# Optimization experiments

Measured on AMD Instinct MI355X. Metric: run time of the kernel, lower is better.

The kernel has to match this reference:

```python
import jax, jax.numpy as jnp
import numpy as np

D = 1024
H = 16
HD = D // H
B = 4
N = 2048


def setup_inputs() -> dict:
    key = jax.random.key(0)
    ks = jax.random.split(key, 5)
    x = jax.random.normal(ks[0], (B, N, D), dtype=jnp.float32)
    # nn.Linear(D, 3D): weight [3D, D], bias [3D]; y = x @ W.T + b
    w_qkv = jax.random.normal(ks[1], (3 * D, D), dtype=jnp.float32) * (1.0 / np.sqrt(D))
    b_qkv = jax.random.normal(ks[2], (3 * D,), dtype=jnp.float32) * 0.02
    w_out = jax.random.normal(ks[3], (D, D), dtype=jnp.float32) * (1.0 / np.sqrt(D))
    b_out = jax.random.normal(ks[4], (D,), dtype=jnp.float32) * 0.02
    return {"x": x, "w_qkv": w_qkv, "b_qkv": b_qkv, "w_out": w_out, "b_out": b_out}


def reference(x, w_qkv, b_qkv, w_out, b_out):
    Bn, Nn, Dn = x.shape
    scale = HD ** (-0.5)
    qkv = x @ w_qkv.T + b_qkv                      # [B, N, 3D]
    q, k, v = jnp.split(qkv, 3, axis=-1)
    # [B, N, D] -> [B, H, N, HD]
    def heads(t):
        return t.reshape(Bn, Nn, H, HD).transpose(0, 2, 1, 3)
    q, k, v = heads(q), heads(k), heads(v)
    scores = jnp.einsum('bhqd,bhkd->bhqk', q, k) * scale   # [B, H, N, N]
    causal = jnp.tril(jnp.ones((Nn, Nn), dtype=bool))
    scores = jnp.where(causal[None, None], scores, jnp.float32(-jnp.inf))
    alpha = jax.nn.softmax(scores, axis=-1)
    out = jnp.einsum('bhqk,bhkd->bhqd', alpha, v)          # [B, H, N, HD]
    out = out.transpose(0, 2, 1, 3).reshape(Bn, Nn, Dn)
    return out @ w_out.T + b_out
```

## Files before the change

### kernel.cpp

```cpp
#include <hip/hip_runtime.h>
#include <hip/hip_bf16.h>

#define D_MODEL 1024
#define H_HEADS 16
#define HD 64
#define B_BATCH 4
#define N_SEQ 2048
#define BH (B_BATCH*H_HEADS)
#define M_TOT (B_BATCH*N_SEQ)
#define N_QKV (3*D_MODEL)
#define QSCALE 0.18033688011112042f

typedef __bf16 bf16x8 __attribute__((ext_vector_type(8)));
typedef __bf16 bf16x4 __attribute__((ext_vector_type(4)));
typedef float f32x4 __attribute__((ext_vector_type(4)));

#define MFMA16 __builtin_amdgcn_mfma_f32_16x16x32_bf16

__device__ inline ushort cvt_bf16(float f){
  return __builtin_bit_cast(ushort, (__bf16)f);
}

#define GLOAD_LDS16(g, l) __builtin_amdgcn_global_load_lds( \
    (const __attribute__((address_space(1))) void*)(g), \
    (__attribute__((address_space(3))) void*)(l), 16, 0, 0)

__global__ void cvt_f32_bf16_kernel(const float* __restrict__ src, ushort* __restrict__ dst, int n){
  int i = (blockIdx.x*blockDim.x + threadIdx.x)*4;
  int stride = gridDim.x*blockDim.x*4;
  for (; i < n; i += stride){
    float4 f = *reinterpret_cast<const float4*>(src+i);
    ushort4 u;
    u.x=cvt_bf16(f.x); u.y=cvt_bf16(f.y); u.z=cvt_bf16(f.z); u.w=cvt_bf16(f.w);
    *reinterpret_cast<ushort4*>(dst+i) = u;
  }
}

template<int MODE>
__global__ __launch_bounds__(512,2) void gemm8p(
    const ushort* __restrict__ A, const ushort* __restrict__ Wt,
    const float* __restrict__ bias, void* __restrict__ out,
    int M, int Ncols, int K)
{
  constexpr int BM=128, BN=256, BK=64;
  __shared__ __align__(16) ushort As[2][2][BM/2][64];
  __shared__ __align__(16) ushort Bs[2][2][BN/2][64];
  const int tid = threadIdx.x;
  const int w = tid>>6, lane = tid&63;
  const int wm = w>>2, wn = w&3;
  const int row0 = blockIdx.y*BM, col0 = blockIdx.x*BN;
  const int lr = lane&15, lk = lane>>4;
  const int s_r   = lane>>3;
  const int c_log = (lane&7) ^ s_r;
  const int g_dr  = (c_log>>2);
  const int g_dc  = (c_log&3)*8;
  const int rdc   = (((lr&1)*4 + lk) ^ ((lr>>1)&7)) * 8;
  f32x4 acc[4][4] = {};

  auto stageA = [&](int buf, int kt, int ks){
    GLOAD_LDS16(&A[(size_t)(row0 + 2*(w*8+s_r) + g_dr)*K + kt*BK + ks*32 + g_dc],
                &As[buf][ks][w*8][0]);
  };
  auto stageB = [&](int buf, int kt, int ks, int u){
    GLOAD_LDS16(&Wt[(size_t)(col0 + u*128 + 2*(w*8+s_r) + g_dr)*K + kt*BK + ks*32 + g_dc],
                &Bs[buf][ks][u*64 + w*8][0]);
  };

  const int NT = K/BK;
  stageA(0,0,0); stageB(0,0,0,0); stageB(0,0,0,1);
  stageA(0,0,1); stageB(0,0,1,0); stageB(0,0,1,1);
  asm volatile("s_waitcnt vmcnt(3)" ::: "memory");
  __builtin_amdgcn_s_barrier();

  int cur = 0;
  for (int kt=0; kt<NT; ++kt){
    const bool last = (kt == NT-1);
    const int nb = cur^1;
    bf16x8 af[4], bfr[2];

    #pragma unroll
    for (int m=0;m<4;m++)
      af[m] = *reinterpret_cast<const bf16x8*>(&As[cur][0][wm*32 + m*8 + (lr>>1)][rdc]);
    bfr[0] = *reinterpret_cast<const bf16x8*>(&Bs[cur][0][wn*32 + 0  + (lr>>1)][rdc]);
    bfr[1] = *reinterpret_cast<const bf16x8*>(&Bs[cur][0][wn*32 + 8  + (lr>>1)][rdc]);
    if (!last){ stageA(nb, kt+1, 0); stageB(nb, kt+1, 0, 0); }
    __builtin_amdgcn_s_barrier();
    asm volatile("s_waitcnt lgkmcnt(0)" ::: "memory");
    __builtin_amdgcn_sched_barrier(0);
    __builtin_amdgcn_s_setprio(1);
    #pragma unroll
    for (int m=0;m<4;m++){
      acc[m][0] = MFMA16(af[m], bfr[0], acc[m][0], 0,0,0);
      acc[m][1] = MFMA16(af[m], bfr[1], acc[m][1], 0,0,0);
    }
    __builtin_amdgcn_s_setprio(0);
    __builtin_amdgcn_s_barrier();

    bfr[0] = *reinterpret_cast<const bf16x8*>(&Bs[cur][0][wn*32 + 16 + (lr>>1)][rdc]);
    bfr[1] = *reinterpret_cast<const bf16x8*>(&Bs[cur][0][wn*32 + 24 + (lr>>1)][rdc]);
    if (!last){ stageB(nb, kt+1, 0, 1); stageA(nb, kt+1, 1); }
    __builtin_amdgcn_s_barrier();
    asm volatile("s_waitcnt lgkmcnt(0)" ::: "memory");
    __builtin_amdgcn_sched_barrier(0);
    __builtin_amdgcn_s_setprio(1);
    #pragma unroll
    for (int m=0;m<4;m++){
      acc[m][2] = MFMA16(af[m], bfr[0], acc[m][2], 0,0,0);
      acc[m][3] = MFMA16(af[m], bfr[1], acc[m][3], 0,0,0);
    }
    __builtin_amdgcn_s_setprio(0);
    if (last) asm volatile("s_waitcnt vmcnt(0)" ::: "memory");
    else      asm volatile("s_waitcnt vmcnt(4)" ::: "memory");
    __builtin_amdgcn_s_barrier();

    #pragma unroll
    for (int m=0;m<4;m++)
      af[m] = *reinterpret_cast<const bf16x8*>(&As[cur][1][wm*32 + m*8 + (lr>>1)][rdc]);
    bfr[0] = *reinterpret_cast<const bf16x8*>(&Bs[cur][1][wn*32 + 0  + (lr>>1)][rdc]);
    bfr[1] = *reinterpret_cast<const bf16x8*>(&Bs[cur][1][wn*32 + 8  + (lr>>1)][rdc]);
    if (!last) stageB(nb, kt+1, 1, 0);
    __builtin_amdgcn_s_barrier();
    asm volatile("s_waitcnt lgkmcnt(0)" ::: "memory");
    __builtin_amdgcn_sched_barrier(0);
    __builtin_amdgcn_s_setprio(1);
    #pragma unroll
    for (int m=0;m<4;m++){
      acc[m][0] = MFMA16(af[m], bfr[0], acc[m][0], 0,0,0);
      acc[m][1] = MFMA16(af[m], bfr[1], acc[m][1], 0,0,0);
    }
    __builtin_amdgcn_s_setprio(0);
    __builtin_amdgcn_s_barrier();

    bfr[0] = *reinterpret_cast<const bf16x8*>(&Bs[cur][1][wn*32 + 16 + (lr>>1)][rdc]);
    bfr[1] = *reinterpret_cast<const bf16x8*>(&Bs[cur][1][wn*32 + 24 + (lr>>1)][rdc]);
    if (!last) stageB(nb, kt+1, 1, 1);
    __builtin_amdgcn_s_barrier();
    asm volatile("s_waitcnt lgkmcnt(0)" ::: "memory");
    __builtin_amdgcn_sched_barrier(0);
    __builtin_amdgcn_s_setprio(1);
    #pragma unroll
    for (int m=0;m<4;m++){
      acc[m][2] = MFMA16(af[m], bfr[0], acc[m][2], 0,0,0);
      acc[m][3] = MFMA16(af[m], bfr[1], acc[m][3], 0,0,0);
    }
    __builtin_amdgcn_s_setprio(0);
    if (!last) asm volatile("s_waitcnt vmcnt(3)" ::: "memory");
    __builtin_amdgcn_s_barrier();
    cur ^= 1;
  }

  const int orow_base = row0 + wm*64;
  const int ocol_base = col0 + wn*64;
  #pragma unroll
  for (int m=0;m<4;m++){
    #pragma unroll
    for(int n=0;n<4;n++){
      const int gc = ocol_base + n*16 + lr;
      const float bv = bias[gc];
      const int gr0 = orow_base + m*16 + lk*4;
      float vals[4];
      #pragma unroll
      for (int r=0;r<4;r++) vals[r] = acc[m][n][r] + bv;
      if (MODE==0){
        const int which = gc >> 10;
        const int d = gc & 1023;
        const int h = d >> 6, hd = d & 63;
        const int b = gr0 >> 11, nn0 = gr0 & 2047;
        ushort* o = (ushort*)out;
        if (which==2){
          ushort4 u;
          u.x=cvt_bf16(vals[0]); u.y=cvt_bf16(vals[1]);
          u.z=cvt_bf16(vals[2]); u.w=cvt_bf16(vals[3]);
          *reinterpret_cast<ushort4*>(
            &o[2ull*BH*N_SEQ*HD + ((size_t)(b*H_HEADS+h)*HD + hd)*N_SEQ + nn0]) = u;
        } else {
          const float sc = (which==0) ? QSCALE : 1.0f;
          #pragma unroll
          for (int r=0;r<4;r++)
            o[(size_t)which*((size_t)BH*N_SEQ*HD)
              + ((size_t)(b*H_HEADS+h)*N_SEQ + nn0 + r)*HD + hd] = cvt_bf16(vals[r]*sc);
        }
      } else {
        #pragma unroll
        for (int r=0;r<4;r++)
          ((float*)out)[(size_t)(gr0+r)*Ncols + gc] = vals[r];
      }
    }
  }
}

__global__ __launch_bounds__(256,3) void attn_mfma(
    const ushort* __restrict__ q, const ushort* __restrict__ kg, const ushort* __restrict__ vtg,
    ushort* __restrict__ attn_out)
{
  __shared__ __align__(16) ushort Ks[2][64][64];
  __shared__ __align__(16) ushort Vs[2][64][64];
  __shared__ __align__(16) ushort Ps[4][32][72];
  const int tid=threadIdx.x, w=tid>>6, lane=tid&63;
  const int lr=lane&15, lk=lane>>4;
  const int bid = blockIdx.x;
  const int strip = 15 - (bid>>6);
  const int bh = bid & 63;
  const size_t base=(size_t)bh*N_SEQ*HD;
  const ushort* kb = kg + base;
  const ushort* vb = vtg + base;
  const int b = bh>>4, h = bh&15;

  const int s_roff = lane>>3;
  const int s_g    = (lane&7) ^ s_roff;
  int rd_base[2];
  #pragma unroll
  for (int ks=0;ks<2;ks++)
    rd_base[ks] = lr*64 + (((ks*4+lk) ^ (lr&7))*8);

  const int row0 = strip*128;
  const int wrow = row0 + w*32;
  const int nt = 2*strip + 2;

  bf16x8 qf[2][2];
  #pragma unroll
  for (int qt=0;qt<2;qt++)
    #pragma unroll
    for (int ks=0;ks<2;ks++)
      qf[qt][ks] = *reinterpret_cast<const bf16x8*>(
          &q[base + (size_t)(wrow + qt*16 + lr)*HD + ks*32 + lk*8]);

  f32x4 o_acc[2][4] = {};
  float mrun[2] = {-1e30f,-1e30f}, lrun[2] = {0.f,0.f};

  {
    const int r0k = w*16, rA = r0k + s_roff;
    GLOAD_LDS16(&kb[(size_t)(rA)*HD + s_g*8],       &Ks[0][r0k][0]);
    GLOAD_LDS16(&kb[(size_t)(rA+8)*HD + s_g*8],     &Ks[0][r0k+8][0]);
    GLOAD_LDS16(&vb[(size_t)(rA)*N_SEQ + s_g*8],    &Vs[0][r0k][0]);
    GLOAD_LDS16(&vb[(size_t)(rA+8)*N_SEQ + s_g*8],  &Vs[0][r0k+8][0]);
  }
  int cur = 0;
  for (int t=0;t<nt;t++){
    __syncthreads();
    if (t+1 < nt){
      const int j1 = (t+1)*64;
      const int r0k = w*16, rA = r0k + s_roff;
      GLOAD_LDS16(&kb[(size_t)(j1+rA)*HD + s_g*8],        &Ks[cur^1][r0k][0]);
      GLOAD_LDS16(&kb[(size_t)(j1+rA+8)*HD + s_g*8],      &Ks[cur^1][r0k+8][0]);
      GLOAD_LDS16(&vb[(size_t)(rA)*N_SEQ + j1 + s_g*8],   &Vs[cur^1][r0k][0]);
      GLOAD_LDS16(&vb[(size_t)(rA+8)*N_SEQ + j1 + s_g*8], &Vs[cur^1][r0k+8][0]);
    }
    const int j0 = t*64;
    if (j0 <= wrow + 31){
      const ushort* Kt = &Ks[cur][0][0];
      const ushort* Vt = &Vs[cur][0][0];
      f32x4 sacc[2][4] = {};
      __builtin_amdgcn_s_setprio(1);
      #pragma unroll
      for (int ks=0;ks<2;ks++)
        #pragma unroll
        for (int kt=0;kt<4;kt++){
          bf16x8 kf = *reinterpret_cast<const bf16x8*>(Kt + kt*1024 + rd_base[ks]);
          sacc[0][kt] = MFMA16(kf, qf[0][ks], sacc[0][kt], 0,0,0);
          sacc[1][kt] = MFMA16(kf, qf[1][ks], sacc[1][kt], 0,0,0);
        }
      __builtin_amdgcn_s_setprio(0);

      const bool tailmask = (j0 + 63 > wrow);
      #pragma unroll
      for (int qt=0;qt<2;qt++){
        const int qrow = wrow + qt*16 + lr;
        if (tailmask){
          #pragma unroll
          for (int kt=0;kt<4;kt++)
            #pragma unroll
            for (int r=0;r<4;r++)
              if (j0 + kt*16 + lk*4 + r > qrow) sacc[qt][kt][r] = -1e30f;
        }
        float mx = -1e30f;
        #pragma unroll
        for (int kt=0;kt<4;kt++)
          #pragma unroll
          for (int r=0;r<4;r++) mx = fmaxf(mx, sacc[qt][kt][r]);
        mx = fmaxf(mx, __shfl_xor(mx, 16));
        mx = fmaxf(mx, __shfl_xor(mx, 32));
        float mcur = mrun[qt];
        if (__any(mx - mcur > 8.0f)){
          const float mnew = fmaxf(mcur, mx);
          const float corr = exp2f(mcur - mnew);
          mrun[qt] = mnew; mcur = mnew;
          lrun[qt] *= corr;
          #pragma unroll
          for (int dt=0;dt<4;dt++) o_acc[qt][dt] *= corr;
        }
        float sum = 0.f;
        #pragma unroll
        for (int kt=0;kt<4;kt++){
          float p0 = exp2f(sacc[qt][kt][0]-mcur);
          float p1 = exp2f(sacc[qt][kt][1]-mcur);
          float p2 = exp2f(sacc[qt][kt][2]-mcur);
          float p3 = exp2f(sacc[qt][kt][3]-mcur);
          sum += (p0+p1)+(p2+p3);
          bf16x4 pk;
          pk[0]=(__bf16)p0; pk[1]=(__bf16)p1; pk[2]=(__bf16)p2; pk[3]=(__bf16)p3;
          *reinterpret_cast<bf16x4*>(&Ps[w][qt*16+lr][kt*16+lk*4]) = pk;
        }
        lrun[qt] += sum;
      }

      #pragma unroll
      for (int ks=0;ks<2;ks++){
        bf16x8 pa0 = *reinterpret_cast<const bf16x8*>(&Ps[w][lr][ks*32+lk*8]);
        bf16x8 pa1 = *reinterpret_cast<const bf16x8*>(&Ps[w][16+lr][ks*32+lk*8]);
        __builtin_amdgcn_s_setprio(1);
        #pragma unroll
        for (int dt=0;dt<4;dt++){
          bf16x8 vf = *reinterpret_cast<const bf16x8*>(Vt + dt*1024 + rd_base[ks]);
          o_acc[0][dt] = MFMA16(vf, pa0, o_acc[0][dt], 0,0,0);
          o_acc[1][dt] = MFMA16(vf, pa1, o_acc[1][dt], 0,0,0);
        }
        __builtin_amdgcn_s_setprio(0);
      }
    }
    cur ^= 1;
  }

  #pragma unroll
  for (int qt=0;qt<2;qt++){
    float rl = lrun[qt];
    rl += __shfl_xor(rl, 16);
    rl += __shfl_xor(rl, 32);
    const float rinv = 1.0f / rl;
    const size_t rowb = ((size_t)(b*N_SEQ) + wrow + qt*16 + lr)*D_MODEL + h*HD;
    #pragma unroll
    for (int dt=0;dt<4;dt++){
      bf16x4 u;
      u[0]=(__bf16)(o_acc[qt][dt][0]*rinv);
      u[1]=(__bf16)(o_acc[qt][dt][1]*rinv);
      u[2]=(__bf16)(o_acc[qt][dt][2]*rinv);
      u[3]=(__bf16)(o_acc[qt][dt][3]*rinv);
      *reinterpret_cast<bf16x4*>(&attn_out[rowb + dt*16 + lk*4]) = u;
    }
  }
}

extern "C" void kernel_launch(void* const* d_in, const int* in_sizes, int n_in,
                              void* d_out, int out_size, void* d_ws, size_t ws_size,
                              hipStream_t stream){
  const float* x     = (const float*)d_in[0];
  const float* w_qkv = (const float*)d_in[1];
  const float* b_qkv = (const float*)d_in[2];
  const float* w_out = (const float*)d_in[3];
  const float* b_out = (const float*)d_in[4];

  char* ws = (char*)d_ws;
  size_t off = 0;
  ushort* x_bf    = (ushort*)(ws+off); off += (size_t)M_TOT*D_MODEL*2;
  ushort* wqkv_bf = (ushort*)(ws+off); off += (size_t)N_QKV*D_MODEL*2;
  ushort* wout_bf = (ushort*)(ws+off); off += (size_t)D_MODEL*D_MODEL*2;
  ushort* qkv     = (ushort*)(ws+off); off += 3ull*BH*N_SEQ*HD*2;
  ushort* attn_o  = (ushort*)(ws+off); off += (size_t)M_TOT*D_MODEL*2;

  cvt_f32_bf16_kernel<<<1024, 256, 0, stream>>>(x,     x_bf,    M_TOT*D_MODEL);
  cvt_f32_bf16_kernel<<<512,  256, 0, stream>>>(w_qkv, wqkv_bf, N_QKV*D_MODEL);
  cvt_f32_bf16_kernel<<<256,  256, 0, stream>>>(w_out, wout_bf, D_MODEL*D_MODEL);

  dim3 g1(N_QKV/256, M_TOT/128);
  gemm8p<0><<<g1, 512, 0, stream>>>(x_bf, wqkv_bf, b_qkv, qkv, M_TOT, N_QKV, D_MODEL);

  const ushort* qb  = qkv;
  const ushort* kb  = qkv + (size_t)BH*N_SEQ*HD;
  const ushort* vtb = qkv + 2ull*BH*N_SEQ*HD;
  attn_mfma<<<1024, 256, 0, stream>>>(qb, kb, vtb, attn_o);

  dim3 g3(D_MODEL/256, M_TOT/128);
  gemm8p<2><<<g3, 512, 0, stream>>>(attn_o, wout_bf, b_out, (float*)d_out, M_TOT, D_MODEL, D_MODEL);
}
```

Measured before the change: 195.4 us.

## Restructure GEMM into deeper-prefetch pipeline with larger tiles and XCD-aware block remap

Replaces the GEMM kernel with a templated version whose M tile is configurable (256 rows for QKV, 128 for output projection). Stores are reissued so loads for K-tile kt+2 go into the buffer just consumed, giving a two-tile prefetch depth. A 1D grid is remapped so consecutive tiles land on the same XCD, improving L2 reuse. Launch bounds drop to one block per CU, trading occupancy for more accumulators and register pressure.

Result: faster. 189.0 us (-3.3%).

```diff
diff --git a/kernel.cpp b/kernel.cpp
--- a/kernel.cpp
+++ b/kernel.cpp
@@ -36,128 +36,142 @@
   }
 }
 
-template<int MODE>
-__global__ __launch_bounds__(512,2) void gemm8p(
+template<int MODE, int MR>
+__global__ __launch_bounds__(512,1) void gemm4p(
     const ushort* __restrict__ A, const ushort* __restrict__ Wt,
     const float* __restrict__ bias, void* __restrict__ out,
     int M, int Ncols, int K)
 {
-  constexpr int BM=128, BN=256, BK=64;
-  __shared__ __align__(16) ushort As[2][2][BM/2][64];
-  __shared__ __align__(16) ushort Bs[2][2][BN/2][64];
+  constexpr int BM = MR*32;
+  constexpr int BN = 256;
+  constexpr int A_SR = BM/2;
+  constexpr int A_ISS = BM/128;
+  constexpr int VN = 2*A_ISS + 2;
+  __shared__ __align__(16) ushort As[2][2][A_SR][64];
+  __shared__ __align__(16) ushort Bs[2][2][128][64];
   const int tid = threadIdx.x;
   const int w = tid>>6, lane = tid&63;
   const int wm = w>>2, wn = w&3;
-  const int row0 = blockIdx.y*BM, col0 = blockIdx.x*BN;
   const int lr = lane&15, lk = lane>>4;
-  const int s_r   = lane>>3;
-  const int c_log = (lane&7) ^ s_r;
-  const int g_dr  = (c_log>>2);
-  const int g_dc  = (c_log&3)*8;
-  const int rdc   = (((lr&1)*4 + lk) ^ ((lr>>1)&7)) * 8;
-  f32x4 acc[4][4] = {};
+
+  const int nx = Ncols/BN;
+  const int q8 = gridDim.x>>3;
+  const int gid = (blockIdx.x&7)*q8 + (blockIdx.x>>3);
+  const int bx = gid % nx, by = gid / nx;
+  const int row0 = by*BM, col0 = bx*BN;
+
+  const int s_sr8 = lane>>3;
+  const int s_cl  = (lane&7) ^ s_sr8;
+  const int s_dr  = s_cl>>2;
+  const int s_dc  = (s_cl&3)*8;
 
   auto stageA = [&](int buf, int kt, int ks){
-    GLOAD_LDS16(&A[(size_t)(row0 + 2*(w*8+s_r) + g_dr)*K + kt*BK + ks*32 + g_dc],
-                &As[buf][ks][w*8][0]);
+    #pragma unroll
+    for (int i=0;i<A_ISS;i++){
+      const int sr0 = (w*A_ISS + i)*8;
+      GLOAD_LDS16(&A[(size_t)(row0 + 2*(sr0 + s_sr8) + s_dr)*K + kt*64 + ks*32 + s_dc],
+                  &As[buf][ks][sr0][0]);
+    }
   };
-  auto stageB = [&](int buf, int kt, int ks, int u){
-    GLOAD_LDS16(&Wt[(size_t)(col0 + u*128 + 2*(w*8+s_r) + g_dr)*K + kt*BK + ks*32 + g_dc],
-                &Bs[buf][ks][u*64 + w*8][0]);
+  auto stageB = [&](int buf, int kt, int ks){
+    #pragma unroll
+    for (int i=0;i<2;i++){
+      const int sr0 = (w*2 + i)*8;
+      GLOAD_LDS16(&Wt[(size_t)(col0 + 2*(sr0 + s_sr8) + s_dr)*K + kt*64 + ks*32 + s_dc],
+                  &Bs[buf][ks][sr0][0]);
+    }
   };
 
-  const int NT = K/BK;
-  stageA(0,0,0); stageB(0,0,0,0); stageB(0,0,0,1);
-  stageA(0,0,1); stageB(0,0,1,0); stageB(0,0,1,1);
-  asm volatile("s_waitcnt vmcnt(3)" ::: "memory");
+  const int rdc = (((lr&1)*4 + lk) ^ ((lr>>1)&7)) * 8;
+  f32x4 acc[MR][4] = {};
+
+  const int NT = K/64;
+  stageA(0,0,0); stageB(0,0,0); stageA(0,0,1); stageB(0,0,1);
+  stageA(1,1,0); stageB(1,1,0); stageA(1,1,1);
+  asm volatile("s_waitcnt vmcnt(%0)" :: "i"(VN) : "memory");
   __builtin_amdgcn_s_barrier();
 
-  int cur = 0;
   for (int kt=0; kt<NT; ++kt){
-    const bool last = (kt == NT-1);
-    const int nb = cur^1;
-    bf16x8 af[4], bfr[2];
-
-    #pragma unroll
-    for (int m=0;m<4;m++)
-      af[m] = *reinterpret_cast<const bf16x8*>(&As[cur][0][wm*32 + m*8 + (lr>>1)][rdc]);
-    bfr[0] = *reinterpret_cast<const bf16x8*>(&Bs[cur][0][wn*32 + 0  + (lr>>1)][rdc]);
-    bfr[1] = *reinterpret_cast<const bf16x8*>(&Bs[cur][0][wn*32 + 8  + (lr>>1)][rdc]);
-    if (!last){ stageA(nb, kt+1, 0); stageB(nb, kt+1, 0, 0); }
+    const int cur = kt&1, nb = cur^1;
+    bf16x8 af[MR], bfr[2];
+
+    #pragma unroll
+    for (int m=0;m<MR;m++)
+      af[m] = *reinterpret_cast<const bf16x8*>(&As[cur][0][wm*(MR*8) + m*8 + (lr>>1)][rdc]);
+    bfr[0] = *reinterpret_cast<const bf16x8*>(&Bs[cur][0][wn*32 + 0*8 + (lr>>1)][rdc]);
+    bfr[1] = *reinterpret_cast<const bf16x8*>(&Bs[cur][0][wn*32 + 1*8 + (lr>>1)][rdc]);
+    if (kt+1 < NT) stageB(nb, kt+1, 1);
     __builtin_amdgcn_s_barrier();
     asm volatile("s_waitcnt lgkmcnt(0)" ::: "memory");
     __builtin_amdgcn_sched_barrier(0);
     __builtin_amdgcn_s_setprio(1);
     #pragma unroll
-    for (int m=0;m<4;m++){
+    for (int m=0;m<MR;m++){
       acc[m][0] = MFMA16(af[m], bfr[0], acc[m][0], 0,0,0);
       acc[m][1] = MFMA16(af[m], bfr[1], acc[m][1], 0,0,0);
     }
     __builtin_amdgcn_s_setprio(0);
     __builtin_amdgcn_s_barrier();
 
-    bfr[0] = *reinterpret_cast<const bf16x8*>(&Bs[cur][0][wn*32 + 16 + (lr>>1)][rdc]);
-    bfr[1] = *reinterpret_cast<const bf16x8*>(&Bs[cur][0][wn*32 + 24 + (lr>>1)][rdc]);
-    if (!last){ stageB(nb, kt+1, 0, 1); stageA(nb, kt+1, 1); }
+    bfr[0] = *reinterpret_cast<const bf16x8*>(&Bs[cur][0][wn*32 + 2*8 + (lr>>1)][rdc]);
+    bfr[1] = *reinterpret_cast<const bf16x8*>(&Bs[cur][0][wn*32 + 3*8 + (lr>>1)][rdc]);
+    if (kt+2 < NT) stageA(cur, kt+2, 0);
     __builtin_amdgcn_s_barrier();
     asm volatile("s_waitcnt lgkmcnt(0)" ::: "memory");
     __builtin_amdgcn_sched_barrier(0);
     __builtin_amdgcn_s_setprio(1);
     #pragma unroll
-    for (int m=0;m<4;m++){
+    for (int m=0;m<MR;m++){
       acc[m][2] = MFMA16(af[m], bfr[0], acc[m][2], 0,0,0);
       acc[m][3] = MFMA16(af[m], bfr[1], acc[m][3], 0,0,0);
     }
     __builtin_amdgcn_s_setprio(0);
-    if (last) asm volatile("s_waitcnt vmcnt(0)" ::: "memory");
-    else      asm volatile("s_waitcnt vmcnt(4)" ::: "memory");
-    __builtin_amdgcn_s_barrier();
-
-    #pragma unroll
-    for (int m=0;m<4;m++)
-      af[m] = *reinterpret_cast<const bf16x8*>(&As[cur][1][wm*32 + m*8 + (lr>>1)][rdc]);
-    bfr[0] = *reinterpret_cast<const bf16x8*>(&Bs[cur][1][wn*32 + 0  + (lr>>1)][rdc]);
-    bfr[1] = *reinterpret_cast<const bf16x8*>(&Bs[cur][1][wn*32 + 8  + (lr>>1)][rdc]);
-    if (!last) stageB(nb, kt+1, 1, 0);
+    __builtin_amdgcn_s_barrier();
+
+    #pragma unroll
+    for (int m=0;m<MR;m++)
+      af[m] = *reinterpret_cast<const bf16x8*>(&As[cur][1][wm*(MR*8) + m*8 + (lr>>1)][rdc]);
+    bfr[0] = *reinterpret_cast<const bf16x8*>(&Bs[cur][1][wn*32 + 0*8 + (lr>>1)][rdc]);
+    bfr[1] = *reinterpret_cast<const bf16x8*>(&Bs[cur][1][wn*32 + 1*8 + (lr>>1)][rdc]);
+    if (kt+2 < NT) stageB(cur, kt+2, 0);
     __builtin_amdgcn_s_barrier();
     asm volatile("s_waitcnt lgkmcnt(0)" ::: "memory");
     __builtin_amdgcn_sched_barrier(0);
     __builtin_amdgcn_s_setprio(1);
     #pragma unroll
-    for (int m=0;m<4;m++){
+    for (int m=0;m<MR;m++){
       acc[m][0] = MFMA16(af[m], bfr[0], acc[m][0], 0,0,0);
       acc[m][1] = MFMA16(af[m], bfr[1], acc[m][1], 0,0,0);
     }
     __builtin_amdgcn_s_setprio(0);
     __builtin_amdgcn_s_barrier();
 
-    bfr[0] = *reinterpret_cast<const bf16x8*>(&Bs[cur][1][wn*32 + 16 + (lr>>1)][rdc]);
-    bfr[1] = *reinterpret_cast<const bf16x8*>(&Bs[cur][1][wn*32 + 24 + (lr>>1)][rdc]);
-    if (!last) stageB(nb, kt+1, 1, 1);
+    bfr[0] = *reinterpret_cast<const bf16x8*>(&Bs[cur][1][wn*32 + 2*8 + (lr>>1)][rdc]);
+    bfr[1] = *reinterpret_cast<const bf16x8*>(&Bs[cur][1][wn*32 + 3*8 + (lr>>1)][rdc]);
+    if (kt+2 < NT) stageA(cur, kt+2, 1);
     __builtin_amdgcn_s_barrier();
     asm volatile("s_waitcnt lgkmcnt(0)" ::: "memory");
     __builtin_amdgcn_sched_barrier(0);
     __builtin_amdgcn_s_setprio(1);
     #pragma unroll
-    for (int m=0;m<4;m++){
+    for (int m=0;m<MR;m++){
       acc[m][2] = MFMA16(af[m], bfr[0], acc[m][2], 0,0,0);
       acc[m][3] = MFMA16(af[m], bfr[1], acc[m][3], 0,0,0);
     }
     __builtin_amdgcn_s_setprio(0);
-    if (!last) asm volatile("s_waitcnt vmcnt(3)" ::: "memory");
-    __builtin_amdgcn_s_barrier();
-    cur ^= 1;
-  }
-
-  const int orow_base = row0 + wm*64;
+    if (kt < NT-2) asm volatile("s_waitcnt vmcnt(%0)" :: "i"(VN) : "memory");
+    else           asm volatile("s_waitcnt vmcnt(0)" ::: "memory");
+    __builtin_amdgcn_s_barrier();
+  }
+
   const int ocol_base = col0 + wn*64;
   #pragma unroll
-  for (int m=0;m<4;m++){
+  for (int m=0;m<MR;m++){
     #pragma unroll
     for(int n=0;n<4;n++){
       const int gc = ocol_base + n*16 + lr;
       const float bv = bias[gc];
-      const int gr0 = orow_base + m*16 + lk*4;
+      const int gr0 = row0 + wm*(MR*16) + m*16 + lk*4;
       float vals[4];
       #pragma unroll
       for (int r=0;r<4;r++) vals[r] = acc[m][n][r] + bv;
@@ -361,14 +375,12 @@
   cvt_f32_bf16_kernel<<<512,  256, 0, stream>>>(w_qkv, wqkv_bf, N_QKV*D_MODEL);
   cvt_f32_bf16_kernel<<<256,  256, 0, stream>>>(w_out, wout_bf, D_MODEL*D_MODEL);
 
-  dim3 g1(N_QKV/256, M_TOT/128);
-  gemm8p<0><<<g1, 512, 0, stream>>>(x_bf, wqkv_bf, b_qkv, qkv, M_TOT, N_QKV, D_MODEL);
+  gemm4p<0,8><<<384, 512, 0, stream>>>(x_bf, wqkv_bf, b_qkv, qkv, M_TOT, N_QKV, D_MODEL);
 
   const ushort* qb  = qkv;
   const ushort* kb  = qkv + (size_t)BH*N_SEQ*HD;
   const ushort* vtb = qkv + 2ull*BH*N_SEQ*HD;
   attn_mfma<<<1024, 256, 0, stream>>>(qb, kb, vtb, attn_o);
 
-  dim3 g3(D_MODEL/256, M_TOT/128);
-  gemm8p<2><<<g3, 512, 0, stream>>>(attn_o, wout_bf, b_out, (float*)d_out, M_TOT, D_MODEL, D_MODEL);
-}
+  gemm4p<2,4><<<256, 512, 0, stream>>>(attn_o, wout_bf, b_out, (float*)d_out, M_TOT, D_MODEL, D_MODEL);
+}
```
